# Kernel tuning notes

Hardware: AMD Instinct MI355X
Metric: run time of the kernel (lower is better)

Reference implementation:

```python
import jax, jax.numpy as jnp
import numpy as np

ACOSH_MIN = 1.0 + 1e-07
ACOSH_MAX = 50.0
TEMP_EPS = 1e-08


def setup_inputs() -> dict:
    key = jax.random.key(0)
    k1, k2 = jax.random.split(key)
    B, S, D = 8, 2048, 65  # manifold_dim = dim + 1 for hyperbolic (Lorentz)
    x = jax.random.normal(k1, (B, S, D), dtype=jnp.float32)
    values = jax.random.normal(k2, (B, S, D), dtype=jnp.float32)
    temperature = jnp.float32(1.0)  # nn.Parameter initialized to 1.0
    return {"x": x, "values": values, "temperature": temperature}


def reference(x, values, temperature):
    # Lorentz (hyperbolic) pairwise inner product:
    # <x_i, x_j>_L = -x_i[0]*x_j[0] + sum_k x_i[k]*x_j[k], k>=1
    time_product = -jnp.einsum('bs,bt->bst', x[..., 0], x[..., 0])
    space_product = jnp.einsum('bsd,btd->bst', x[..., 1:], x[..., 1:])
    lorentz_product = time_product + space_product  # [B,S,S]
    acosh_input = jnp.clip(-lorentz_product, ACOSH_MIN, ACOSH_MAX)
    distances = jnp.arccosh(acosh_input)
    scores = -distances / (temperature + TEMP_EPS)
    attention = jax.nn.softmax(scores, axis=-1)  # [B,S,S]
    output = jnp.einsum('bst,btd->bsd', attention, values)
    return (output, attention)
```

## Files before the change

### kernel.cpp

```cpp
#include <hip/hip_runtime.h>
#include <math.h>

constexpr int NB = 8, NS = 2048, ND = 65;
constexpr int KX = 64;
constexpr int LP = 68;
constexpr int VD = 80;
constexpr size_t OUTSZ = (size_t)NB * NS * ND;
constexpr size_t CONVN = (size_t)NB * NS * KX;
constexpr size_t VTN   = (size_t)NB * VD * NS;

typedef short short8 __attribute__((ext_vector_type(8)));
typedef float f32x4 __attribute__((ext_vector_type(4)));

union S8U { short8 v; ushort4 h[2]; };
__device__ __forceinline__ short8 ld8(const ushort* p) {
    S8U u; u.h[0] = *(const ushort4*)p; u.h[1] = *(const ushort4*)(p + 4); return u.v;
}

__device__ __forceinline__ ushort f2bf(float f) {
    uint u = __float_as_uint(f);
    return (ushort)((u + 0x7fffu + ((u >> 16) & 1u)) >> 16);
}
__device__ __forceinline__ float bf2f(ushort h) {
    return __uint_as_float((uint)h << 16);
}

__global__ __launch_bounds__(256)
void k0_convert(const float* __restrict__ x, ushort* __restrict__ xhi,
                ushort* __restrict__ xlo, float* __restrict__ x64)
{
    int i = blockIdx.x * 256 + threadIdx.x;
    int row = i >> 3, g = i & 7;
    if (row >= NB * NS) return;
    int d0 = g * 8;
    short8 vh, vl;
    #pragma unroll
    for (int e = 0; e < 8; ++e) {
        float v = x[(size_t)row * ND + d0 + e];
        ushort h = f2bf(v);
        vh[e] = (short)h;
        vl[e] = (short)f2bf(v - bf2f(h));
    }
    *(short8*)&xhi[(size_t)row * KX + d0] = vh;
    *(short8*)&xlo[(size_t)row * KX + d0] = vl;
    if (g == 0) x64[row] = x[(size_t)row * ND + 64];
}

__global__ __launch_bounds__(256)
void k0v_transpose(const float* __restrict__ v, ushort* __restrict__ vthi)
{
    __shared__ float sT[32][66];
    const int tid = threadIdx.x, b = blockIdx.y, t0 = blockIdx.x * 32;
    const float* vb = v + (size_t)b * NS * ND;
    for (int i = tid; i < 32 * ND; i += 256) {
        int t = i / ND, d = i - t * ND;
        sT[t][d] = vb[(size_t)(t0 + t) * ND + d];
    }
    __syncthreads();
    for (int i = tid; i < VD * 32; i += 256) {
        int d = i >> 5, t = i & 31;
        float val = (d < ND) ? sT[t][d] : 0.0f;
        vthi[((size_t)b * VD + d) * NS + t0 + t] = f2bf(val);
    }
}

__global__ __launch_bounds__(512, 4)
void k1u_scores(const ushort* __restrict__ xhi, const ushort* __restrict__ xlo,
                const float* __restrict__ x64, const float* __restrict__ tptr,
                ushort* __restrict__ eg, float* __restrict__ invb)
{
    __shared__ __align__(16) ushort sAh[64 * LP], sAl[64 * LP];
    __shared__ __align__(16) ushort sBh[128 * LP], sBl[128 * LP];
    __shared__ __align__(16) float sB64[128];

    const int tid = threadIdx.x;
    const int f  = (blockIdx.x & 7) * 32 + (blockIdx.x >> 3);
    const int b  = f >> 5;
    const int r0 = (f & 31) * 64;
    const int lane = tid & 63;
    const int q = lane >> 4, c = lane & 15;
    const int w  = tid >> 6;
    const int wr = w >> 2;
    const int wc = w & 3;
    const float invT = 1.0f / (tptr[0] + 1e-8f);
    const bool fastT = (invT == 1.0f);

    const ushort* xhb = xhi + (size_t)b * NS * KX;
    const ushort* xlb = xlo + (size_t)b * NS * KX;
    const float*  x64b = x64 + (size_t)b * NS;
    ushort* erow = eg + ((size_t)b * NS + r0) * NS;

    for (int i = tid; i < 64 * 8; i += 512) {
        int row = i >> 3, g = i & 7;
        uint4 vh = *(const uint4*)&xhb[(size_t)(r0 + row) * KX + g * 8];
        uint4 vl = *(const uint4*)&xlb[(size_t)(r0 + row) * KX + g * 8];
        int so = row * LP + g * 8;
        *(uint2*)&sAh[so]     = make_uint2(vh.x, vh.y);
        *(uint2*)&sAh[so + 4] = make_uint2(vh.z, vh.w);
        *(uint2*)&sAl[so]     = make_uint2(vl.x, vl.y);
        *(uint2*)&sAl[so + 4] = make_uint2(vl.z, vl.w);
    }
    __syncthreads();
    if (tid < 64) { sAh[tid * LP] ^= 0x8000; sAl[tid * LP] ^= 0x8000; }

    float a64r[2];
    #pragma unroll
    for (int rf = 0; rf < 2; ++rf)
        a64r[rf] = x64b[r0 + wr * 32 + rf * 16 + c];

    float rsum[2] = {0.0f, 0.0f};

    for (int tc = 0; tc < NS; tc += 128) {
        __syncthreads();
        for (int i = tid; i < 128 * 8; i += 512) {
            int row = i >> 3, g = i & 7;
            uint4 vh = *(const uint4*)&xhb[(size_t)(tc + row) * KX + g * 8];
            uint4 vl = *(const uint4*)&xlb[(size_t)(tc + row) * KX + g * 8];
            int so = row * LP + g * 8;
            *(uint2*)&sBh[so]     = make_uint2(vh.x, vh.y);
            *(uint2*)&sBh[so + 4] = make_uint2(vh.z, vh.w);
            *(uint2*)&sBl[so]     = make_uint2(vl.x, vl.y);
            *(uint2*)&sBl[so + 4] = make_uint2(vl.z, vl.w);
        }
        if (tid < 128) sB64[tid] = x64b[tc + tid];
        __syncthreads();

        f32x4 acc[2][2];
        #pragma unroll
        for (int rf = 0; rf < 2; ++rf)
            #pragma unroll
            for (int cf = 0; cf < 2; ++cf)
                #pragma unroll
                for (int j = 0; j < 4; ++j) acc[rf][cf][j] = 0.0f;

        #pragma unroll
        for (int kc = 0; kc < 2; ++kc) {
            const int koff = kc * 32 + q * 8;
            short8 ah[2], al[2], bh[2], bl[2];
            #pragma unroll
            for (int rf = 0; rf < 2; ++rf) {
                int ro = (wr * 32 + rf * 16 + c) * LP + koff;
                ah[rf] = ld8(&sAh[ro]);
                al[rf] = ld8(&sAl[ro]);
            }
            #pragma unroll
            for (int cf = 0; cf < 2; ++cf) {
                int co = (wc * 32 + cf * 16 + c) * LP + koff;
                bh[cf] = ld8(&sBh[co]);
                bl[cf] = ld8(&sBl[co]);
            }
            #pragma unroll
            for (int rf = 0; rf < 2; ++rf)
                #pragma unroll
                for (int cf = 0; cf < 2; ++cf) {
                    acc[rf][cf] = __builtin_amdgcn_mfma_f32_16x16x32_bf16(bh[cf], ah[rf], acc[rf][cf], 0, 0, 0);
                    acc[rf][cf] = __builtin_amdgcn_mfma_f32_16x16x32_bf16(bl[cf], ah[rf], acc[rf][cf], 0, 0, 0);
                    acc[rf][cf] = __builtin_amdgcn_mfma_f32_16x16x32_bf16(bh[cf], al[rf], acc[rf][cf], 0, 0, 0);
                }
        }

        #pragma unroll
        for (int rf = 0; rf < 2; ++rf) {
            const int row = wr * 32 + rf * 16 + c;
            #pragma unroll
            for (int cf = 0; cf < 2; ++cf) {
                float4 b64v = *(const float4*)&sB64[wc * 32 + cf * 16 + q * 4];
                float e4[4];
                #pragma unroll
                for (int j = 0; j < 4; ++j) {
                    float bj = (j == 0) ? b64v.x : (j == 1) ? b64v.y
                             : (j == 2) ? b64v.z : b64v.w;
                    float accf = acc[rf][cf][j] + a64r[rf] * bj;
                    float z = -accf;
                    z = fminf(fmaxf(z, 1.0000001f), 50.0f);
                    float s = __fsqrt_rn(z * z - 1.0f);
                    float e = fastT ? (z - s)
                                    : __expf(-__logf(z + s) * invT);
                    e4[j] = e;
                    rsum[rf] += e;
                }
                ushort4 pk = make_ushort4(
                    (ushort)__float2uint_rn(e4[0] * 65535.0f),
                    (ushort)__float2uint_rn(e4[1] * 65535.0f),
                    (ushort)__float2uint_rn(e4[2] * 65535.0f),
                    (ushort)__float2uint_rn(e4[3] * 65535.0f));
                *(ushort4*)&erow[(size_t)row * NS + tc + wc * 32 + cf * 16 + q * 4] = pk;
            }
        }
    }

    __syncthreads();
    float* sSum = (float*)sBh;
    #pragma unroll
    for (int rf = 0; rf < 2; ++rf) {
        float v = rsum[rf];
        v += __shfl_xor(v, 16, 64);
        v += __shfl_xor(v, 32, 64);
        if (q == 0) sSum[wc * 64 + wr * 32 + rf * 16 + c] = v;
    }
    __syncthreads();
    if (tid < 64)
        invb[(size_t)b * NS + r0 + tid] =
            1.0f / (sSum[tid] + sSum[64 + tid] + sSum[128 + tid] + sSum[192 + tid]);
}

__global__ __launch_bounds__(256, 4)
void k2u_pv(const ushort* __restrict__ eg, const ushort* __restrict__ vthi,
            const float* __restrict__ invb, float* __restrict__ attn,
            float* __restrict__ out)
{
    __shared__ __align__(16) char smem[40960];
    ushort* sAh = (ushort*)smem;
    ushort* sAl = sAh + 32 * 136;
    ushort* sVh = sAl + 32 * 136;
    float*  sInvL = (float*)(smem + 39168);
    float*  sRed = (float*)smem;

    const int tid = threadIdx.x;
    const int f  = (blockIdx.x & 7) * 64 + (blockIdx.x >> 3);
    const int b  = f >> 6;
    const int r0 = (f & 63) * 32;
    const int lane = tid & 63;
    const int wk = tid >> 6;

    if (tid < 32) sInvL[tid] = invb[(size_t)b * NS + r0 + tid] * (1.0f / 65535.0f);

    const ushort* erow = eg + ((size_t)b * NS + r0) * NS;
    float* arow = attn + ((size_t)b * NS + r0) * NS;
    const ushort* vh = vthi + (size_t)b * VD * NS;

    short8 ereg[2];
    short8 vregh[5];
    auto loadE = [&](int kt) {
        #pragma unroll
        for (int rep = 0; rep < 2; ++rep) {
            int idx = tid + rep * 256;
            int row = idx >> 4, c8 = idx & 15;
            ereg[rep] = *(const short8*)&erow[(size_t)row * NS + kt + c8 * 8];
        }
    };
    auto loadV = [&](int kt) {
        #pragma unroll
        for (int rep = 0; rep < 5; ++rep) {
            int i = tid + rep * 256;
            int d = i >> 4, c8 = i & 15;
            vregh[rep] = *(const short8*)&vh[(size_t)d * NS + kt + c8 * 8];
        }
    };

    f32x4 acc[2][5];
    #pragma unroll
    for (int rf = 0; rf < 2; ++rf)
        #pragma unroll
        for (int ff = 0; ff < 5; ++ff)
            #pragma unroll
            for (int j = 0; j < 4; ++j) acc[rf][ff][j] = 0.0f;

    loadE(0);
    loadV(0);
    __syncthreads();

    for (int kt = 0; kt < NS; kt += 128) {
        #pragma unroll
        for (int rep = 0; rep < 2; ++rep) {
            int idx = tid + rep * 256;
            int row = idx >> 4, c8 = idx & 15;
            float inv2 = sInvL[row];
            float en[8];
            #pragma unroll
            for (int i = 0; i < 8; ++i)
                en[i] = (float)(ushort)ereg[rep][i] * inv2;
            float4 fa = {en[0], en[1], en[2], en[3]};
            float4 fb = {en[4], en[5], en[6], en[7]};
            *(float4*)&arow[(size_t)row * NS + kt + c8 * 8]     = fa;
            *(float4*)&arow[(size_t)row * NS + kt + c8 * 8 + 4] = fb;
            ushort h[8], l[8];
            #pragma unroll
            for (int i = 0; i < 8; ++i) {
                h[i] = f2bf(en[i]);
                l[i] = f2bf(en[i] - bf2f(h[i]));
            }
            int so = row * 136 + c8 * 8;
            *(ushort4*)&sAh[so]     = make_ushort4(h[0], h[1], h[2], h[3]);
            *(ushort4*)&sAh[so + 4] = make_ushort4(h[4], h[5], h[6], h[7]);
            *(ushort4*)&sAl[so]     = make_ushort4(l[0], l[1], l[2], l[3]);
            *(ushort4*)&sAl[so + 4] = make_ushort4(l[4], l[5], l[6], l[7]);
        }
        #pragma unroll
        for (int rep = 0; rep < 5; ++rep) {
            int i = tid + rep * 256;
            int d = i >> 4, c8 = i & 15;
            *(short8*)&sVh[d * 136 + c8 * 8] = vregh[rep];
        }
        __syncthreads();

        if (kt + 128 < NS) { loadE(kt + 128); loadV(kt + 128); }

        const int koff = wk * 32 + (lane >> 4) * 8;
        short8 ah[2], al[2];
        #pragma unroll
        for (int rf = 0; rf < 2; ++rf) {
            int ro = (rf * 16 + (lane & 15)) * 136 + koff;
            ah[rf] = *(const short8*)&sAh[ro];
            al[rf] = *(const short8*)&sAl[ro];
        }
        #pragma unroll
        for (int ff = 0; ff < 5; ++ff) {
            short8 bh = *(const short8*)&sVh[(ff * 16 + (lane & 15)) * 136 + koff];
            #pragma unroll
            for (int rf = 0; rf < 2; ++rf) {
                acc[rf][ff] = __builtin_amdgcn_mfma_f32_16x16x32_bf16(ah[rf], bh, acc[rf][ff], 0, 0, 0);
                acc[rf][ff] = __builtin_amdgcn_mfma_f32_16x16x32_bf16(al[rf], bh, acc[rf][ff], 0, 0, 0);
            }
        }
        __syncthreads();
    }

    #pragma unroll
    for (int rf = 0; rf < 2; ++rf)
        #pragma unroll
        for (int ff = 0; ff < 5; ++ff)
            #pragma unroll
            for (int j = 0; j < 4; ++j) {
                int r = rf * 16 + (lane >> 4) * 4 + j;
                int d = ff * 16 + (lane & 15);
                sRed[((size_t)wk * 32 + r) * 80 + d] = acc[rf][ff][j];
            }
    __syncthreads();
    for (int i = tid; i < 32 * 80; i += 256) {
        int r = i / 80, d = i - r * 80;
        float s = sRed[(size_t)r * 80 + d] + sRed[(size_t)(32 + r) * 80 + d]
                + sRed[(size_t)(64 + r) * 80 + d] + sRed[(size_t)(96 + r) * 80 + d];
        if (d < ND) out[((size_t)b * NS + r0 + r) * ND + d] = s;
    }
}

extern "C" void kernel_launch(void* const* d_in, const int* in_sizes, int n_in,
                              void* d_out, int out_size, void* d_ws, size_t ws_size,
                              hipStream_t stream) {
    const float* x      = (const float*)d_in[0];
    const float* values = (const float*)d_in[1];
    const float* temp   = (const float*)d_in[2];

    float* out  = (float*)d_out;
    float* attn = out + OUTSZ;

    ushort* xhi  = (ushort*)d_ws;
    ushort* xlo  = xhi + CONVN;
    ushort* vthi = xlo + CONVN;
    float*  x64  = (float*)(vthi + VTN);
    float*  invb = x64 + (size_t)NB * NS;
    ushort* eg   = (ushort*)(invb + (size_t)NB * NS);

    k0_convert<<<(NB * NS * 8) / 256, 256, 0, stream>>>(x, xhi, xlo, x64);
    k0v_transpose<<<dim3(NS / 32, NB), 256, 0, stream>>>(values, vthi);

    k1u_scores<<<256, 512, 0, stream>>>(xhi, xlo, x64, temp, eg, invb);
    k2u_pv<<<512, 256, 0, stream>>>(eg, vthi, invb, attn, out);
}
```

Measured before the change: 93.60 us.

## Split score kernel over key halves and widen PV kernel to 512 threads

The score kernel now splits each 64-row block's key range into two halves, doubling its grid from 256 to 512 blocks. Each half writes a partial row sum, and a new small kernel adds the two halves and inverts them. The PV kernel goes to 512 threads per block, with each wave owning one 16-row fragment instead of two, so fewer accumulators are held per thread and more waves run. The costs are an extra kernel launch, a workspace round-trip for the partial sums, and a heavier per-block register and LDS budget in the PV kernel.

Result: faster. 82.15 us (-12.2%).

```diff
diff --git a/kernel.cpp b/kernel.cpp
--- a/kernel.cpp
+++ b/kernel.cpp
@@ -67,16 +67,19 @@
 __global__ __launch_bounds__(512, 4)
 void k1u_scores(const ushort* __restrict__ xhi, const ushort* __restrict__ xlo,
                 const float* __restrict__ x64, const float* __restrict__ tptr,
-                ushort* __restrict__ eg, float* __restrict__ invb)
+                ushort* __restrict__ eg, float* __restrict__ rsp)
 {
     __shared__ __align__(16) ushort sAh[64 * LP], sAl[64 * LP];
     __shared__ __align__(16) ushort sBh[128 * LP], sBl[128 * LP];
     __shared__ __align__(16) float sB64[128];
 
     const int tid = threadIdx.x;
-    const int f  = (blockIdx.x & 7) * 32 + (blockIdx.x >> 3);
-    const int b  = f >> 5;
-    const int r0 = (f & 31) * 64;
+    const int f  = (blockIdx.x & 7) * 64 + (blockIdx.x >> 3);
+    const int b  = f >> 6;
+    const int rblk = (f >> 1) & 31;
+    const int ch = f & 1;
+    const int r0 = rblk * 64;
+    const int tc0 = ch * (NS / 2);
     const int lane = tid & 63;
     const int q = lane >> 4, c = lane & 15;
     const int w  = tid >> 6;
@@ -110,7 +113,8 @@
 
     float rsum[2] = {0.0f, 0.0f};
 
-    for (int tc = 0; tc < NS; tc += 128) {
+    for (int tcl = 0; tcl < NS / 2; tcl += 128) {
+        const int tc = tc0 + tcl;
         __syncthreads();
         for (int i = tid; i < 128 * 8; i += 512) {
             int row = i >> 3, g = i & 7;
@@ -200,11 +204,18 @@
     }
     __syncthreads();
     if (tid < 64)
-        invb[(size_t)b * NS + r0 + tid] =
-            1.0f / (sSum[tid] + sSum[64 + tid] + sSum[128 + tid] + sSum[192 + tid]);
-}
-
-__global__ __launch_bounds__(256, 4)
+        rsp[(size_t)ch * NB * NS + (size_t)b * NS + r0 + tid] =
+            sSum[tid] + sSum[64 + tid] + sSum[128 + tid] + sSum[192 + tid];
+}
+
+__global__ __launch_bounds__(256)
+void k1b_inv(const float* __restrict__ rsp, float* __restrict__ invb)
+{
+    int i = blockIdx.x * 256 + threadIdx.x;
+    invb[i] = 1.0f / (rsp[i] + rsp[(size_t)NB * NS + i]);
+}
+
+__global__ __launch_bounds__(512, 4)
 void k2u_pv(const ushort* __restrict__ eg, const ushort* __restrict__ vthi,
             const float* __restrict__ invb, float* __restrict__ attn,
             float* __restrict__ out)
@@ -221,7 +232,10 @@
     const int b  = f >> 6;
     const int r0 = (f & 63) * 32;
     const int lane = tid & 63;
-    const int wk = tid >> 6;
+    const int q = lane >> 4, c = lane & 15;
+    const int w = tid >> 6;
+    const int wk = w & 3;
+    const int rfh = w >> 2;
 
     if (tid < 32) sInvL[tid] = invb[(size_t)b * NS + r0 + tid] * (1.0f / 65535.0f);
 
@@ -229,47 +243,41 @@
     float* arow = attn + ((size_t)b * NS + r0) * NS;
     const ushort* vh = vthi + (size_t)b * VD * NS;
 
-    short8 ereg[2];
-    short8 vregh[5];
+    short8 ereg;
+    short8 vregh[3];
     auto loadE = [&](int kt) {
-        #pragma unroll
-        for (int rep = 0; rep < 2; ++rep) {
-            int idx = tid + rep * 256;
-            int row = idx >> 4, c8 = idx & 15;
-            ereg[rep] = *(const short8*)&erow[(size_t)row * NS + kt + c8 * 8];
-        }
+        int row = tid >> 4, c8 = tid & 15;
+        ereg = *(const short8*)&erow[(size_t)row * NS + kt + c8 * 8];
     };
     auto loadV = [&](int kt) {
         #pragma unroll
-        for (int rep = 0; rep < 5; ++rep) {
-            int i = tid + rep * 256;
-            int d = i >> 4, c8 = i & 15;
-            vregh[rep] = *(const short8*)&vh[(size_t)d * NS + kt + c8 * 8];
+        for (int rep = 0; rep < 3; ++rep) {
+            int i = tid + rep * 512;
+            if (i < VD * 16) {
+                int d = i >> 4, c8 = i & 15;
+                vregh[rep] = *(const short8*)&vh[(size_t)d * NS + kt + c8 * 8];
+            }
         }
     };
 
-    f32x4 acc[2][5];
-    #pragma unroll
-    for (int rf = 0; rf < 2; ++rf)
-        #pragma unroll
-        for (int ff = 0; ff < 5; ++ff)
-            #pragma unroll
-            for (int j = 0; j < 4; ++j) acc[rf][ff][j] = 0.0f;
+    f32x4 acc[5];
+    #pragma unroll
+    for (int ff = 0; ff < 5; ++ff)
+        #pragma unroll
+        for (int j = 0; j < 4; ++j) acc[ff][j] = 0.0f;
 
     loadE(0);
     loadV(0);
     __syncthreads();
 
     for (int kt = 0; kt < NS; kt += 128) {
-        #pragma unroll
-        for (int rep = 0; rep < 2; ++rep) {
-            int idx = tid + rep * 256;
-            int row = idx >> 4, c8 = idx & 15;
+        {
+            int row = tid >> 4, c8 = tid & 15;
             float inv2 = sInvL[row];
             float en[8];
             #pragma unroll
             for (int i = 0; i < 8; ++i)
-                en[i] = (float)(ushort)ereg[rep][i] * inv2;
+                en[i] = (float)(ushort)ereg[i] * inv2;
             float4 fa = {en[0], en[1], en[2], en[3]};
             float4 fb = {en[4], en[5], en[6], en[7]};
             *(float4*)&arow[(size_t)row * NS + kt + c8 * 8]     = fa;
@@ -287,50 +295,41 @@
             *(ushort4*)&sAl[so + 4] = make_ushort4(l[4], l[5], l[6], l[7]);
         }
         #pragma unroll
-        for (int rep = 0; rep < 5; ++rep) {
-            int i = tid + rep * 256;
-            int d = i >> 4, c8 = i & 15;
-            *(short8*)&sVh[d * 136 + c8 * 8] = vregh[rep];
+        for (int rep = 0; rep < 3; ++rep) {
+            int i = tid + rep * 512;
+            if (i < VD * 16) {
+                int d = i >> 4, c8 = i & 15;
+                *(short8*)&sVh[d * 136 + c8 * 8] = vregh[rep];
+            }
         }
         __syncthreads();
 
         if (kt + 128 < NS) { loadE(kt + 128); loadV(kt + 128); }
 
-        const int koff = wk * 32 + (lane >> 4) * 8;
-        short8 ah[2], al[2];
-        #pragma unroll
-        for (int rf = 0; rf < 2; ++rf) {
-            int ro = (rf * 16 + (lane & 15)) * 136 + koff;
-            ah[rf] = *(const short8*)&sAh[ro];
-            al[rf] = *(const short8*)&sAl[ro];
-        }
+        const int koff = wk * 32 + q * 8;
+        short8 ah = *(const short8*)&sAh[(rfh * 16 + c) * 136 + koff];
+        short8 al = *(const short8*)&sAl[(rfh * 16 + c) * 136 + koff];
         #pragma unroll
         for (int ff = 0; ff < 5; ++ff) {
-            short8 bh = *(const short8*)&sVh[(ff * 16 + (lane & 15)) * 136 + koff];
-            #pragma unroll
-            for (int rf = 0; rf < 2; ++rf) {
-                acc[rf][ff] = __builtin_amdgcn_mfma_f32_16x16x32_bf16(ah[rf], bh, acc[rf][ff], 0, 0, 0);
-                acc[rf][ff] = __builtin_amdgcn_mfma_f32_16x16x32_bf16(al[rf], bh, acc[rf][ff], 0, 0, 0);
-            }
+            short8 bh = *(const short8*)&sVh[(ff * 16 + c) * 136 + koff];
+            acc[ff] = __builtin_amdgcn_mfma_f32_16x16x32_bf16(ah, bh, acc[ff], 0, 0, 0);
+            acc[ff] = __builtin_amdgcn_mfma_f32_16x16x32_bf16(al, bh, acc[ff], 0, 0, 0);
         }
         __syncthreads();
     }
 
     #pragma unroll
-    for (int rf = 0; rf < 2; ++rf)
-        #pragma unroll
-        for (int ff = 0; ff < 5; ++ff)
-            #pragma unroll
-            for (int j = 0; j < 4; ++j) {
-                int r = rf * 16 + (lane >> 4) * 4 + j;
-                int d = ff * 16 + (lane & 15);
-                sRed[((size_t)wk * 32 + r) * 80 + d] = acc[rf][ff][j];
-            }
-    __syncthreads();
-    for (int i = tid; i < 32 * 80; i += 256) {
+    for (int ff = 0; ff < 5; ++ff)
+        #pragma unroll
+        for (int j = 0; j < 4; ++j) {
+            int r = rfh * 16 + q * 4 + j;
+            int d = ff * 16 + c;
+            sRed[((size_t)wk * 32 + r) * 80 + d] = acc[ff][j];
+        }
+    __syncthreads();
+    for (int i = tid; i < 32 * 80; i += 512) {
         int r = i / 80, d = i - r * 80;
-        float s = sRed[(size_t)r * 80 + d] + sRed[(size_t)(32 + r) * 80 + d]
-                + sRed[(size_t)(64 + r) * 80 + d] + sRed[(size_t)(96 + r) * 80 + d];
+        float s = sRed[i] + sRed[2560 + i] + sRed[5120 + i] + sRed[7680 + i];
         if (d < ND) out[((size_t)b * NS + r0 + r) * ND + d] = s;
     }
 }
@@ -350,11 +349,13 @@
     ushort* vthi = xlo + CONVN;
     float*  x64  = (float*)(vthi + VTN);
     float*  invb = x64 + (size_t)NB * NS;
-    ushort* eg   = (ushort*)(invb + (size_t)NB * NS);
+    float*  rsp  = invb + (size_t)NB * NS;
+    ushort* eg   = (ushort*)(rsp + 2 * (size_t)NB * NS);
 
     k0_convert<<<(NB * NS * 8) / 256, 256, 0, stream>>>(x, xhi, xlo, x64);
     k0v_transpose<<<dim3(NS / 32, NB), 256, 0, stream>>>(values, vthi);
 
-    k1u_scores<<<256, 512, 0, stream>>>(xhi, xlo, x64, temp, eg, invb);
-    k2u_pv<<<512, 256, 0, stream>>>(eg, vthi, invb, attn, out);
-}
+    k1u_scores<<<512, 512, 0, stream>>>(xhi, xlo, x64, temp, eg, rsp);
+    k1b_inv<<<NB * NS / 256, 256, 0, stream>>>(rsp, invb);
+    k2u_pv<<<512, 512, 0, stream>>>(eg, vthi, invb, attn, out);
+}
```
